# Optimization experiments

Hardware: AMD Instinct MI355X
Metric: run time of the kernel (lower is better)

The kernel has to match this reference:

```python
import jax, jax.numpy as jnp
import numpy as np

EPS = 1e-5  # BatchNorm eps (torch default)

def setup_inputs() -> dict:
    key = jax.random.key(0)
    ks = jax.random.split(key, 24)
    B, NX, NY, F = 8, 128, 128, 128
    dims = [2 * F, 512, 256, 128, 64]
    d = {
        'x': jax.random.normal(ks[0], (B, NX, F), dtype=jnp.float32),
        'y': jax.random.normal(ks[1], (B, NY, F), dtype=jnp.float32),
    }
    i = 2
    for li, (din, dout) in enumerate(zip(dims[:-1], dims[1:]), start=1):
        d[f'w{li}'] = jax.random.normal(ks[i], (dout, din), dtype=jnp.float32) * (1.0 / np.sqrt(din)); i += 1
        d[f'b{li}'] = jax.random.normal(ks[i], (dout,), dtype=jnp.float32) * 0.02; i += 1
        if li < 4:  # BatchNorm1d on hidden layers only (eval mode: running stats)
            d[f'g{li}'] = 1.0 + 0.1 * jax.random.normal(ks[i], (dout,), dtype=jnp.float32); i += 1
            d[f'be{li}'] = 0.1 * jax.random.normal(ks[i], (dout,), dtype=jnp.float32); i += 1
            d[f'm{li}'] = 0.1 * jax.random.normal(ks[i], (dout,), dtype=jnp.float32); i += 1
            d[f'v{li}'] = 0.5 + jax.random.uniform(ks[i], (dout,), dtype=jnp.float32); i += 1
    return d

def _bn(h, g, be, m, v):
    # BatchNorm1d in eval mode over the channel (last) axis
    return (h - m) * (g * jax.lax.rsqrt(v + EPS)) + be

def reference(x, y,
              w1, b1, g1, be1, m1, v1,
              w2, b2, g2, be2, m2, v2,
              w3, b3, g3, be3, m3, v3,
              w4, b4):
    F = x.shape[-1]
    # First Linear on cat([x_i, y_j]) == split-weight broadcast add: avoids the
    # (B,nx,ny,2F) pairwise concat the torch code materializes (same math).
    wx, wy = w1[:, :F], w1[:, F:]                      # (512,F) each
    hx = jnp.einsum('bif,hf->bih', x, wx)              # (B,nx,512)
    hy = jnp.einsum('bjf,hf->bjh', y, wy)              # (B,ny,512)
    h = hx[:, :, None, :] + hy[:, None, :, :] + b1     # (B,nx,ny,512)
    h = jax.nn.relu(_bn(h, g1, be1, m1, v1))           # dropout is identity in eval
    h = jax.nn.relu(_bn(jnp.einsum('bijh,oh->bijo', h, w2) + b2, g2, be2, m2, v2))
    h = jax.nn.relu(_bn(jnp.einsum('bijh,oh->bijo', h, w3) + b3, g3, be3, m3, v3))
    e = jnp.einsum('bijh,oh->bijo', h, w4) + b4        # (B,nx,ny,64) embeddings
    # PSD path: einsum('bijk,bilk->bijl', e, e).sum(-1)
    #         == sum_k e[b,i,j,k] * (sum_l e[b,i,l,k])  -- avoids (B,nx,ny,ny)
    s = e.sum(axis=2)                                  # (B,nx,64)
    kernel = jnp.einsum('bijk,bik->bij', e, s)         # (B,nx,ny)
    return kernel
```

## Files before the change

kernel.cpp:

```cpp
#include <hip/hip_runtime.h>

#define EPS 1e-5f

typedef _Float16 half8 __attribute__((ext_vector_type(8)));
typedef _Float16 half4 __attribute__((ext_vector_type(4)));
typedef float f32x16 __attribute__((ext_vector_type(16)));
typedef float f32x4v __attribute__((ext_vector_type(4)));


__global__ __launch_bounds__(256)
void pre_kernel(
    const float* __restrict__ x, const float* __restrict__ y,
    const float* __restrict__ w1, const float* __restrict__ b1,
    const float* __restrict__ g1, const float* __restrict__ be1,
    const float* __restrict__ m1, const float* __restrict__ v1,
    const float* __restrict__ w2, const float* __restrict__ b2,
    const float* __restrict__ g2, const float* __restrict__ be2,
    const float* __restrict__ m2, const float* __restrict__ v2,
    const float* __restrict__ w3, const float* __restrict__ b3,
    const float* __restrict__ g3, const float* __restrict__ be3,
    const float* __restrict__ m3, const float* __restrict__ v3,
    const float* __restrict__ w4,
    _Float16* __restrict__ hxh, _Float16* __restrict__ hyh,
    _Float16* __restrict__ w2h, _Float16* __restrict__ w3h,
    _Float16* __restrict__ w4h,
    float* __restrict__ b2f, float* __restrict__ b3f)
{
    const int t = threadIdx.x;

    if (blockIdx.x >= 256) {
        int tid = (blockIdx.x - 256) * 256 + t;
        const int nth = 64 * 256;
        for (int idx = tid; idx < 256 * 512; idx += nth) {
            int n = idx >> 9, k = idx & 511;
            float a = g2[n] * rsqrtf(v2[n] + EPS);
            int addr = ((n >> 5) * 32 + (k >> 4)) * 512 + ((k >> 3) & 1) * 256 + (n & 31) * 8 + (k & 7);
            w2h[addr] = (_Float16)(a * w2[idx]);
        }
        for (int idx = tid; idx < 128 * 256; idx += nth) {
            int n = idx >> 8, k = idx & 255;
            float a = g3[n] * rsqrtf(v3[n] + EPS);
            int addr = ((n >> 5) * 16 + (k >> 4)) * 512 + ((k >> 3) & 1) * 256 + (n & 31) * 8 + (k & 7);
            w3h[addr] = (_Float16)(a * w3[idx]);
        }
        for (int idx = tid; idx < 64 * 128; idx += nth) {
            int n = idx >> 7, k = idx & 127;
            int addr = ((n >> 5) * 8 + (k >> 4)) * 512 + ((k >> 3) & 1) * 256 + (n & 31) * 8 + (k & 7);
            w4h[addr] = (_Float16)w4[idx];
        }
        if (tid < 256) {
            float a = g2[tid] * rsqrtf(v2[tid] + EPS);
            b2f[tid] = a * b2[tid] + be2[tid] - m2[tid] * a;
        } else if (tid < 384) {
            int n = tid - 256;
            float a = g3[n] * rsqrtf(v3[n] + EPS);
            b3f[n] = a * b3[n] + be3[n] - m3[n] * a;
        }
        return;
    }

    const int rg = blockIdx.x & 31;
    const int ng = (blockIdx.x >> 5) & 3;
    const int which = blockIdx.x >> 7;

    constexpr int LDA = 136;
    __shared__ _Float16 sh[32 * 136 + 128 * 136] __attribute__((aligned(16)));
    _Float16* xa = sh;
    _Float16* wb = sh + 32 * 136;

    const int rowbase = rg * 32;
    const float* src = which ? y : x;

#pragma unroll
    for (int p = 0; p < 4; ++p) {
        int c = p * 256 + t;
        int r = c >> 5, fo = (c & 31) * 4;
        f32x4v v = *(const f32x4v*)(src + (size_t)(rowbase + r) * 128 + fo);
        half4 h; h[0] = (_Float16)v[0]; h[1] = (_Float16)v[1];
        h[2] = (_Float16)v[2]; h[3] = (_Float16)v[3];
        *(half4*)(xa + r * LDA + fo) = h;
    }
#pragma unroll
    for (int p = 0; p < 16; ++p) {
        int c = p * 256 + t;
        int n = c >> 5, fo = (c & 31) * 4;
        f32x4v v = *(const f32x4v*)(w1 + (size_t)(ng * 128 + n) * 256 + which * 128 + fo);
        half4 h; h[0] = (_Float16)v[0]; h[1] = (_Float16)v[1];
        h[2] = (_Float16)v[2]; h[3] = (_Float16)v[3];
        *(half4*)(wb + n * LDA + fo) = h;
    }
    __syncthreads();

    const int wid = t >> 6;
    const int l = t & 63;
    const int l31 = l & 31, lh = l >> 5;

    f32x16 acc = (f32x16)0.f;
#pragma unroll
    for (int kc = 0; kc < 8; ++kc) {
        half8 af = *(const half8*)(xa + l31 * LDA + kc * 16 + lh * 8);
        half8 bf = *(const half8*)(wb + (wid * 32 + l31) * LDA + kc * 16 + lh * 8);
        acc = __builtin_amdgcn_mfma_f32_32x32x16_f16(af, bf, acc, 0, 0, 0);
    }

    const int n = ng * 128 + wid * 32 + l31;
    float alpha = g1[n] * rsqrtf(v1[n] + EPS);
    if (which == 0) {
        float bias = alpha * b1[n] + be1[n] - m1[n] * alpha;
#pragma unroll
        for (int r = 0; r < 16; ++r) {
            int m = (r & 3) + 8 * (r >> 2) + 4 * lh;
            hxh[(size_t)(rowbase + m) * 512 + n] = (_Float16)(alpha * acc[r] + bias);
        }
    } else {
        const int ks = n >> 4, lhh = (n >> 3) & 1, c = n & 7;
#pragma unroll
        for (int r = 0; r < 16; ++r) {
            int m = (r & 3) + 8 * (r >> 2) + 4 * lh;
            int R = rowbase + m;
            int bb = R >> 7, j = R & 127;
            int addr = bb * 65536 + ((j >> 5) * 32 + ks) * 512 + lhh * 256 + (j & 31) * 8 + c;
            hyh[addr] = (_Float16)(alpha * acc[r]);
        }
    }
}

__global__ __launch_bounds__(1024, 4)
void fused_kernel(
    const _Float16* __restrict__ hxh, const _Float16* __restrict__ hyh,
    const _Float16* __restrict__ w2h, const _Float16* __restrict__ w3h,
    const _Float16* __restrict__ w4h,
    const float* __restrict__ b2f, const float* __restrict__ b3f,
    const float* __restrict__ b4,
    float* __restrict__ out)
{
    constexpr int LD2 = 264;
    constexpr int LD3 = 136;
    constexpr int LDE = 68;
    constexpr int REG = 67584;

    __shared__ char smem[8192 + 2 * REG] __attribute__((aligned(16)));
    _Float16* hxs = (_Float16*)smem;
    float* spart  = (float*)(smem + 2048);
    float* ss     = (float*)(smem + 6144);
    char* R1 = smem + 8192;

    const int b  = blockIdx.x >> 6;
    const int ip = blockIdx.x & 63;
    const int i0 = ip * 2;
    const int t = threadIdx.x;
    const int wid = t >> 6;
    const int l   = t & 63;
    const int l31 = l & 31;
    const int lh  = l >> 5;

    if (t < 128) {
        int iv = t >> 6;
        *(half8*)(hxs + iv * 512 + (t & 63) * 8) =
            *(const half8*)(hxh + (size_t)(b * 128 + i0 + iv) * 512 + (t & 63) * 8);
    }
    __syncthreads();

    const int wm = wid >> 2, wn = wid & 3;

    const _Float16* pa  = hyh + (size_t)b * 65536 + (size_t)(wm * 32) * 512 + l * 8;
    const _Float16* pb0 = w2h + (size_t)(2 * wn) * 32 * 512 + l * 8;
    const _Float16* pb1 = pb0 + 32 * 512;

    const float bb0 = b2f[wn * 64 + l31];
    const float bb1 = b2f[wn * 64 + 32 + l31];
    f32x16 d0 = (f32x16)bb0, d1 = (f32x16)bb1;
    f32x16 e0 = (f32x16)bb0, e1 = (f32x16)bb1;

    half8 A0, B00, B01;
    half8 A1, B10, B11;

    auto LD0 = [&](int ks) {
        A0  = *(const half8*)(pa  + (size_t)ks * 512);
        B00 = *(const half8*)(pb0 + (size_t)ks * 512);
        B01 = *(const half8*)(pb1 + (size_t)ks * 512);
    };
    auto LD1 = [&](int ks) {
        A1  = *(const half8*)(pa  + (size_t)ks * 512);
        B10 = *(const half8*)(pb0 + (size_t)ks * 512);
        B11 = *(const half8*)(pb1 + (size_t)ks * 512);
    };
    auto RELU = [&](half8 a, half8 rx) {
        half8 s = a + rx;
        half8 af;
#pragma unroll
        for (int c = 0; c < 8; ++c)
            af[c] = s[c] > (_Float16)0.f ? s[c] : (_Float16)0.f;
        return af;
    };
    auto STEP0 = [&](int ks) {
        half8 rx0 = *(const half8*)(hxs + ks * 16 + lh * 8);
        half8 rx1 = *(const half8*)(hxs + 512 + ks * 16 + lh * 8);
        half8 af = RELU(A0, rx0);
        d0 = __builtin_amdgcn_mfma_f32_32x32x16_f16(af, B00, d0, 0, 0, 0);
        d1 = __builtin_amdgcn_mfma_f32_32x32x16_f16(af, B01, d1, 0, 0, 0);
        af = RELU(A0, rx1);
        e0 = __builtin_amdgcn_mfma_f32_32x32x16_f16(af, B00, e0, 0, 0, 0);
        e1 = __builtin_amdgcn_mfma_f32_32x32x16_f16(af, B01, e1, 0, 0, 0);
    };
    auto STEP1 = [&](int ks) {
        half8 rx0 = *(const half8*)(hxs + ks * 16 + lh * 8);
        half8 rx1 = *(const half8*)(hxs + 512 + ks * 16 + lh * 8);
        half8 af = RELU(A1, rx0);
        d0 = __builtin_amdgcn_mfma_f32_32x32x16_f16(af, B10, d0, 0, 0, 0);
        d1 = __builtin_amdgcn_mfma_f32_32x32x16_f16(af, B11, d1, 0, 0, 0);
        af = RELU(A1, rx1);
        e0 = __builtin_amdgcn_mfma_f32_32x32x16_f16(af, B10, e0, 0, 0, 0);
        e1 = __builtin_amdgcn_mfma_f32_32x32x16_f16(af, B11, e1, 0, 0, 0);
    };

    LD0(0);
#pragma unroll 2
    for (int ks = 0; ks < 32; ks += 2) {
        if (ks + 1 < 32) LD1(ks + 1);
        STEP0(ks);
        if (ks + 2 < 32) LD0(ks + 2);
        if (ks + 1 < 32) STEP1(ks + 1);
    }

    {
        _Float16* a2_0 = (_Float16*)R1;
        _Float16* a2_1 = (_Float16*)(R1 + REG);
#pragma unroll
        for (int r = 0; r < 16; ++r) {
            int m = wm * 32 + (r & 3) + 8 * (r >> 2) + 4 * lh;
            a2_0[m * LD2 + wn * 64 + l31]      = (_Float16)fmaxf(d0[r], 0.f);
            a2_0[m * LD2 + wn * 64 + 32 + l31] = (_Float16)fmaxf(d1[r], 0.f);
            a2_1[m * LD2 + wn * 64 + l31]      = (_Float16)fmaxf(e0[r], 0.f);
            a2_1[m * LD2 + wn * 64 + 32 + l31] = (_Float16)fmaxf(e1[r], 0.f);
        }
    }
    __syncthreads();

    const int team = wid >> 3;
    const int tw   = wid & 7;
    char* reg = R1 + team * REG;
    _Float16* a2 = (_Float16*)reg;
    _Float16* a3 = (_Float16*)reg;
    float*    es = (float*)reg;
    float* spart_t = spart + team * 512;
    float* ss_t    = ss + team * 64;
    const int iv = i0 + team;

    const int wm3 = tw >> 2, wn3 = tw & 3;
    f32x16 g0, g1;
    {
        float b3v = b3f[wn3 * 32 + l31];
        g0 = (f32x16)b3v;
        g1 = (f32x16)b3v;
    }
#pragma unroll 4
    for (int kc = 0; kc < 16; ++kc) {
        half8 bfr = *(const half8*)(w3h + (wn3 * 16 + kc) * 512 + l * 8);
        half8 af0 = *(const half8*)(a2 + (wm3 * 64 + l31) * LD2 + kc * 16 + lh * 8);
        half8 af1 = *(const half8*)(a2 + (wm3 * 64 + 32 + l31) * LD2 + kc * 16 + lh * 8);
        g0 = __builtin_amdgcn_mfma_f32_32x32x16_f16(af0, bfr, g0, 0, 0, 0);
        g1 = __builtin_amdgcn_mfma_f32_32x32x16_f16(af1, bfr, g1, 0, 0, 0);
    }
    __syncthreads();
#pragma unroll
    for (int mt = 0; mt < 2; ++mt)
#pragma unroll
        for (int r = 0; r < 16; ++r) {
            int m = wm3 * 64 + mt * 32 + (r & 3) + 8 * (r >> 2) + 4 * lh;
            a3[m * LD3 + wn3 * 32 + l31] = (_Float16)fmaxf(mt ? g1[r] : g0[r], 0.f);
        }
    __syncthreads();

    const int wm4 = tw >> 1, wn4 = tw & 1;
    f32x16 acc4 = (f32x16)(b4[wn4 * 32 + l31]);
#pragma unroll
    for (int kc = 0; kc < 8; ++kc) {
        half8 afr = *(const half8*)(a3 + (wm4 * 32 + l31) * LD3 + kc * 16 + lh * 8);
        half8 bfr = *(const half8*)(w4h + (wn4 * 8 + kc) * 512 + l * 8);
        acc4 = __builtin_amdgcn_mfma_f32_32x32x16_f16(afr, bfr, acc4, 0, 0, 0);
    }
    __syncthreads();
#pragma unroll
    for (int r = 0; r < 16; ++r) {
        int m = wm4 * 32 + (r & 3) + 8 * (r >> 2) + 4 * lh;
        es[m * LDE + wn4 * 32 + l31] = acc4[r];
    }
    __syncthreads();

    {
        float sv = 0.f;
#pragma unroll
        for (int jj = 0; jj < 16; ++jj) sv += es[(tw + jj * 8) * LDE + l];
        spart_t[tw * 64 + l] = sv;
    }
    __syncthreads();
    if ((t & 511) < 64) {
        int tt = t & 63;
        float s2 = 0.f;
#pragma unroll
        for (int r = 0; r < 8; ++r) s2 += spart_t[r * 64 + tt];
        ss_t[tt] = s2;
    }
    __syncthreads();
    {
        const int tt = t & 511;
        const int j = tt >> 2, q = tt & 3;
        float p = 0.f;
#pragma unroll
        for (int c = 0; c < 16; ++c) {
            int k = q + 4 * c;
            p += es[j * LDE + k] * ss_t[k];
        }
        p += __shfl_xor(p, 1);
        p += __shfl_xor(p, 2);
        if (q == 0) out[(size_t)(b * 128 + iv) * 128 + j] = p;
    }
}

extern "C" void kernel_launch(void* const* d_in, const int* in_sizes, int n_in,
                              void* d_out, int out_size, void* d_ws, size_t ws_size,
                              hipStream_t stream)
{
    (void)in_sizes; (void)n_in; (void)out_size; (void)ws_size;

    const float* x   = (const float*)d_in[0];
    const float* y   = (const float*)d_in[1];
    const float* w1  = (const float*)d_in[2];
    const float* b1  = (const float*)d_in[3];
    const float* g1  = (const float*)d_in[4];
    const float* be1 = (const float*)d_in[5];
    const float* m1  = (const float*)d_in[6];
    const float* v1  = (const float*)d_in[7];
    const float* w2  = (const float*)d_in[8];
    const float* b2  = (const float*)d_in[9];
    const float* g2  = (const float*)d_in[10];
    const float* be2 = (const float*)d_in[11];
    const float* m2  = (const float*)d_in[12];
    const float* v2  = (const float*)d_in[13];
    const float* w3  = (const float*)d_in[14];
    const float* b3  = (const float*)d_in[15];
    const float* g3  = (const float*)d_in[16];
    const float* be3 = (const float*)d_in[17];
    const float* m3  = (const float*)d_in[18];
    const float* v3  = (const float*)d_in[19];
    const float* w4  = (const float*)d_in[20];
    const float* b4  = (const float*)d_in[21];
    float* out = (float*)d_out;

    float* b2f = (float*)d_ws;
    float* b3f = b2f + 256;
    _Float16* w2h = (_Float16*)(b3f + 128);
    _Float16* w3h = w2h + 131072;
    _Float16* w4h = w3h + 32768;
    _Float16* hxh = w4h + 8192;
    _Float16* hyh = hxh + 524288;

    hipLaunchKernelGGL(pre_kernel, dim3(320), dim3(256), 0, stream,
                       x, y, w1, b1, g1, be1, m1, v1,
                       w2, b2, g2, be2, m2, v2,
                       w3, b3, g3, be3, m3, v3,
                       w4,
                       hxh, hyh, w2h, w3h, w4h, b2f, b3f);

    hipLaunchKernelGGL(fused_kernel, dim3(512), dim3(1024), 0, stream,
                       hxh, hyh, w2h, w3h, w4h, b2f, b3f, b4, out);
}
```

Measured before the change: 68.45 us.

## Stage relu(hx+hy) layer-1 activations in shared memory once per block

Layer-1 activations (relu of hy plus hx) used to be recomputed by every wave from hy loaded straight from global memory, so each of the four wn waves redid the same loads and adds. Now each k-chunk of activations is built once cooperatively, written to a double-buffered LDS region, and read back by all waves for the MFMAs, with the next chunk's global load overlapped with the current chunk's compute. This cuts redundant global loads and VALU work, at the cost of a __syncthreads per chunk and extra LDS traffic.

```diff
diff --git a/kernel.cpp b/kernel.cpp
--- a/kernel.cpp
+++ b/kernel.cpp
@@ -144,6 +144,7 @@
     float* spart  = (float*)(smem + 2048);
     float* ss     = (float*)(smem + 6144);
     char* R1 = smem + 8192;
+    _Float16* a1 = (_Float16*)R1;
 
     const int b  = blockIdx.x >> 6;
     const int ip = blockIdx.x & 63;
@@ -161,9 +162,10 @@
     }
     __syncthreads();
 
+    const int srg = wid >> 2, sksl = wid & 3;
+    const _Float16* hysrc = hyh + (size_t)b * 65536
+                          + (size_t)(srg * 32 + sksl) * 512 + l * 8;
     const int wm = wid >> 2, wn = wid & 3;
-
-    const _Float16* pa  = hyh + (size_t)b * 65536 + (size_t)(wm * 32) * 512 + l * 8;
     const _Float16* pb0 = w2h + (size_t)(2 * wn) * 32 * 512 + l * 8;
     const _Float16* pb1 = pb0 + 32 * 512;
 
@@ -172,55 +174,53 @@
     f32x16 d0 = (f32x16)bb0, d1 = (f32x16)bb1;
     f32x16 e0 = (f32x16)bb0, e1 = (f32x16)bb1;
 
-    half8 A0, B00, B01;
-    half8 A1, B10, B11;
-
-    auto LD0 = [&](int ks) {
-        A0  = *(const half8*)(pa  + (size_t)ks * 512);
-        B00 = *(const half8*)(pb0 + (size_t)ks * 512);
-        B01 = *(const half8*)(pb1 + (size_t)ks * 512);
+    half8 hyreg;
+
+    auto SLOAD = [&](int c) {
+        hyreg = *(const half8*)(hysrc + (size_t)c * 4 * 512);
     };
-    auto LD1 = [&](int ks) {
-        A1  = *(const half8*)(pa  + (size_t)ks * 512);
-        B10 = *(const half8*)(pb0 + (size_t)ks * 512);
-        B11 = *(const half8*)(pb1 + (size_t)ks * 512);
+    auto SFIN = [&](int c) {
+        const int ksg = c * 4 + sksl;
+        half8 hx0 = *(const half8*)(hxs + ksg * 16 + lh * 8);
+        half8 hx1 = *(const half8*)(hxs + 512 + ksg * 16 + lh * 8);
+        half8 s0 = hyreg + hx0;
+        half8 s1 = hyreg + hx1;
+        half8 a0, a1f;
+#pragma unroll
+        for (int cc = 0; cc < 8; ++cc) {
+            a0[cc]  = s0[cc] > (_Float16)0.f ? s0[cc] : (_Float16)0.f;
+            a1f[cc] = s1[cc] > (_Float16)0.f ? s1[cc] : (_Float16)0.f;
+        }
+        _Float16* dst = a1 + (size_t)((c & 1) * 32 + srg * 4 + sksl) * 512 + l * 8;
+        *(half8*)dst = a0;
+        *(half8*)(dst + 16 * 512) = a1f;
     };
-    auto RELU = [&](half8 a, half8 rx) {
-        half8 s = a + rx;
-        half8 af;
-#pragma unroll
-        for (int c = 0; c < 8; ++c)
-            af[c] = s[c] > (_Float16)0.f ? s[c] : (_Float16)0.f;
-        return af;
+    auto CONSUME = [&](int c) {
+        const _Float16* ab0 = a1 + (size_t)((c & 1) * 32 + wm * 4) * 512 + l * 8;
+        const _Float16* ab1 = ab0 + 16 * 512;
+#pragma unroll
+        for (int ksl = 0; ksl < 4; ++ksl) {
+            const int ksg = c * 4 + ksl;
+            half8 Ai0 = *(const half8*)(ab0 + ksl * 512);
+            half8 Ai1 = *(const half8*)(ab1 + ksl * 512);
+            half8 Bx  = *(const half8*)(pb0 + (size_t)ksg * 512);
+            half8 By  = *(const half8*)(pb1 + (size_t)ksg * 512);
+            d0 = __builtin_amdgcn_mfma_f32_32x32x16_f16(Ai0, Bx, d0, 0, 0, 0);
+            d1 = __builtin_amdgcn_mfma_f32_32x32x16_f16(Ai0, By, d1, 0, 0, 0);
+            e0 = __builtin_amdgcn_mfma_f32_32x32x16_f16(Ai1, Bx, e0, 0, 0, 0);
+            e1 = __builtin_amdgcn_mfma_f32_32x32x16_f16(Ai1, By, e1, 0, 0, 0);
+        }
     };
-    auto STEP0 = [&](int ks) {
-        half8 rx0 = *(const half8*)(hxs + ks * 16 + lh * 8);
-        half8 rx1 = *(const half8*)(hxs + 512 + ks * 16 + lh * 8);
-        half8 af = RELU(A0, rx0);
-        d0 = __builtin_amdgcn_mfma_f32_32x32x16_f16(af, B00, d0, 0, 0, 0);
-        d1 = __builtin_amdgcn_mfma_f32_32x32x16_f16(af, B01, d1, 0, 0, 0);
-        af = RELU(A0, rx1);
-        e0 = __builtin_amdgcn_mfma_f32_32x32x16_f16(af, B00, e0, 0, 0, 0);
-        e1 = __builtin_amdgcn_mfma_f32_32x32x16_f16(af, B01, e1, 0, 0, 0);
-    };
-    auto STEP1 = [&](int ks) {
-        half8 rx0 = *(const half8*)(hxs + ks * 16 + lh * 8);
-        half8 rx1 = *(const half8*)(hxs + 512 + ks * 16 + lh * 8);
-        half8 af = RELU(A1, rx0);
-        d0 = __builtin_amdgcn_mfma_f32_32x32x16_f16(af, B10, d0, 0, 0, 0);
-        d1 = __builtin_amdgcn_mfma_f32_32x32x16_f16(af, B11, d1, 0, 0, 0);
-        af = RELU(A1, rx1);
-        e0 = __builtin_amdgcn_mfma_f32_32x32x16_f16(af, B10, e0, 0, 0, 0);
-        e1 = __builtin_amdgcn_mfma_f32_32x32x16_f16(af, B11, e1, 0, 0, 0);
-    };
-
-    LD0(0);
+
+    SLOAD(0);
+    SFIN(0);
+    __syncthreads();
 #pragma unroll 2
-    for (int ks = 0; ks < 32; ks += 2) {
-        if (ks + 1 < 32) LD1(ks + 1);
-        STEP0(ks);
-        if (ks + 2 < 32) LD0(ks + 2);
-        if (ks + 1 < 32) STEP1(ks + 1);
+    for (int c = 0; c < 8; ++c) {
+        if (c < 7) SLOAD(c + 1);
+        CONSUME(c);
+        if (c < 7) SFIN(c + 1);
+        __syncthreads();
     }
 
     {
```

Result: faster. 63.37 us (-7.4%).
